# Performance work log

Measured on AMD Instinct MI355X. Metric: run time of the kernel, lower is better.

The kernel has to match this reference:

```python
import jax, jax.numpy as jnp
import numpy as np
import math

C = 16
K = 16
M = 64
DEPTH = 4          # int(sqrt(K)) tree depth
D = C * 9          # input feature dim, 9 dims per codebook subspace
N = 1024 * 128     # rows
N_NODES = K - 1    # 15 internal nodes of a depth-4 binary tree


def _selection_matrix(C):
    # node i at tree level l reads the per-codebook hashed feature at depth index l
    S = np.zeros((C * N_NODES, C * DEPTH), np.float32)
    for c in range(C):
        for i in range(N_NODES):
            level = 0 if i == 0 else (1 if i < 3 else (2 if i < 7 else 3))
            S[c * N_NODES + i, c * DEPTH + level] = 1.0
    return S


def _bit_matrix(C, K):
    # row (c,k): +/-1 on the 4 tree nodes along code k's root-to-leaf path;
    # matching code scores DEPTH, every other code scores <= DEPTH-2
    B = np.zeros((C * K, C * N_NODES), np.float32)
    for c in range(C):
        for k in range(K):
            prefix = 0
            for l in range(DEPTH):
                bit = (k >> (DEPTH - 1 - l)) & 1
                node = (2 ** l - 1) + prefix
                B[c * K + k, c * N_NODES + node] = 1.0 if bit else -1.0
                prefix = prefix * 2 + bit
    return B


def setup_inputs() -> dict:
    key = jax.random.key(0)
    k1, k2, k3, k4 = jax.random.split(key, 4)
    I = jax.random.normal(k1, (N, D), jnp.float32) - 0.5
    A = jax.random.normal(k2, (C, D // C, DEPTH), jnp.float32)   # soft hashing projections
    T = jax.random.normal(k3, (C * N_NODES,), jnp.float32)       # node thresholds
    bound = math.sqrt(1.0 / (C * K))  # kaiming_uniform with a=sqrt(5), fan_in=C*K
    L = jax.random.uniform(k4, (M, C, K), jnp.float32, -bound, bound)  # lookup tables
    S = jnp.asarray(_selection_matrix(C))
    B = jnp.asarray(_bit_matrix(C, K))
    return {"I": I, "A": A, "T": T, "L": L, "S": S, "B": B}


def reference(I, A, T, L, S, B):
    n = I.shape[0]
    # per-codebook soft hash: (n, C, D//C) x (C, D//C, DEPTH) -> (n, C*DEPTH)
    h = jnp.einsum('ncd,cdp->ncp', I.reshape(n, C, D // C), A).reshape(n, C * DEPTH)
    # thresholded tree decisions with straight-through sign
    b = h @ S.T - T                                   # (n, C*15)
    t = jnp.tanh(b)
    s = jax.lax.stop_gradient(jnp.sign(b) - t) + t    # fwd: sign, bwd: tanh'
    # bit-matrix decode of path agreements -> per-code scores
    scores = (s @ B.T).reshape(n, C, K)               # (n, C, K), max DEPTH at true code
    onehot = jax.nn.one_hot(jnp.argmax(scores, axis=2), K, dtype=I.dtype)
    E = jax.lax.stop_gradient(onehot - scores) + scores  # STE one-hot encoding
    # LUT gather-accumulate: out[n,m] = sum_c L[m,c,code(n,c)]
    return jnp.einsum('nck,mck->nm', E, L)
```

## Files before the change

kernel.cpp:

```cpp
#include <hip/hip_runtime.h>
#include <hip/hip_fp16.h>


#define NROWS (1024 * 128)

typedef __attribute__((ext_vector_type(2))) float f32x2;

__global__ __launch_bounds__(256, 2) void halut_fwd(
    const float* __restrict__ I,
    const float* __restrict__ A,
    const float* __restrict__ T,
    const float* __restrict__ L,
    float* __restrict__ out)
{
    __shared__ uint32_t sLut[8192];
    __shared__ float    sStage[4][2304];
    __shared__ uint8_t  sCodes[4096];

    const int tid  = threadIdx.x;
    const int w    = tid >> 6;
    const int lane = tid & 63;

    const int cB = lane & 15;
    const int g  = lane >> 4;
    f32x2 a01[9], a23[9];
    {
        const float4* ap4 = (const float4*)(A + cB * 36);
        #pragma unroll
        for (int i = 0; i < 9; ++i) {
            const float4 v = ap4[i];
            a01[i] = (f32x2){v.x, v.y};
            a23[i] = (f32x2){v.z, v.w};
        }
    }
    float Tf[15];
    #pragma unroll
    for (int j = 0; j < 15; ++j) Tf[j] = T[cB * 15 + j];

    {
        uint4* lut4 = (uint4*)sLut;
        #pragma unroll
        for (int q = 0; q < 8; ++q) {
            uint32_t wv[4];
            #pragma unroll
            for (int e = 0; e < 4; ++e) {
                const float fa = L[(8*q + 2*e)     * 256 + tid];
                const float fb = L[(8*q + 2*e + 1) * 256 + tid];
                wv[e] = ((uint32_t)__half_as_ushort(__float2half_rn(fb)) << 16)
                      |  (uint32_t)__half_as_ushort(__float2half_rn(fa));
            }
            lut4[q * 256 + tid] = make_uint4(wv[0], wv[1], wv[2], wv[3]);
        }
    }
    __syncthreads();

    const int wave_row0 = blockIdx.x * 256 + w * 64;
    const float4* Isrc = (const float4*)I;
    float4* st4 = (float4*)sStage[w];

    float4 nbuf[9];
    #pragma unroll
    for (int i = 0; i < 9; ++i)
        nbuf[i] = Isrc[(size_t)wave_row0 * 36 + i * 64 + lane];

    const int lvl[15] = {0, 1,1, 2,2,2,2, 3,3,3,3,3,3,3,3};

    #pragma unroll
    for (int p16 = 0; p16 < 4; ++p16) {
        #pragma unroll
        for (int i = 0; i < 9; ++i) st4[i * 64 + lane] = nbuf[i];
        if (p16 < 3) {
            #pragma unroll
            for (int i = 0; i < 9; ++i)
                nbuf[i] = Isrc[(size_t)(wave_row0 + (p16+1)*16) * 36 + i*64 + lane];
        }
        #pragma unroll
        for (int ps = 0; ps < 4; ++ps) {
            const int lr = ps * 4 + g;
            const float* xr = &sStage[w][lr * 144 + cB * 9];

            float xv[9];
            f32x2 h01 = (f32x2){0.f, 0.f}, h23 = (f32x2){0.f, 0.f};
            #pragma unroll
            for (int d = 0; d < 9; ++d) {
                const float x = xr[d];
                xv[d] = x;
                const f32x2 xx = (f32x2){x, x};
                h01 = __builtin_elementwise_fma(xx, a01[d], h01);
                h23 = __builtin_elementwise_fma(xx, a23[d], h23);
            }
            const float hh[4] = {h01.x, h01.y, h23.x, h23.y};

            uint32_t mk = 0, bl = 0;
            #pragma unroll
            for (int j = 0; j < 15; ++j) {
                const float b = hh[lvl[j]] - Tf[j];
                mk |= (b > 0.f) ? (1u << j) : 0u;
                bl |= (fabsf(b) < 1e-3f) ? 1u : 0u;
            }
            if (bl) {
                double h0 = 0.0, h1 = 0.0, h2 = 0.0, h3 = 0.0;
                #pragma unroll
                for (int d = 0; d < 9; ++d) {
                    const double x = (double)xv[d];
                    h0 = fma(x, (double)a01[d].x, h0);
                    h1 = fma(x, (double)a01[d].y, h1);
                    h2 = fma(x, (double)a23[d].x, h2);
                    h3 = fma(x, (double)a23[d].y, h3);
                }
                const double hd[4] = {h0, h1, h2, h3};
                mk = 0;
                #pragma unroll
                for (int j = 0; j < 15; ++j)
                    mk |= (hd[lvl[j]] > (double)Tf[j]) ? (1u << j) : 0u;
            }
            int p =       (int)(mk & 1u);
            p = 2 * p + (int)((mk >> (1 + p)) & 1u);
            p = 2 * p + (int)((mk >> (3 + p)) & 1u);
            p = 2 * p + (int)((mk >> (7 + p)) & 1u);
            sCodes[(w * 64 + p16 * 16 + lr) * 16 + cB] = (uint8_t)p;
        }
    }

    const uint4 cw = *(const uint4*)&sCodes[tid * 16];
    const uint32_t cd0 = cw.x, cd1 = cw.y, cd2 = cw.z, cd3 = cw.w;

    __half2 acc2[32];
    #pragma unroll
    for (int k = 0; k < 32; ++k) acc2[k] = __floats2half2_rn(0.f, 0.f);

    const uint4* lut4 = (const uint4*)sLut;
    #pragma unroll 4
    for (int c = 0; c < 16; ++c) {
        const uint32_t cdw = (c < 4) ? cd0 : (c < 8) ? cd1 : (c < 12) ? cd2 : cd3;
        const int p = (int)((cdw >> ((c & 3) * 8)) & 15u);
        const uint4* colp = lut4 + (c << 4) + p;
        #pragma unroll
        for (int q = 0; q < 8; ++q) {
            const uint4 wv = colp[q << 8];
            acc2[q*4+0] = __hadd2(acc2[q*4+0], *(const __half2*)&wv.x);
            acc2[q*4+1] = __hadd2(acc2[q*4+1], *(const __half2*)&wv.y);
            acc2[q*4+2] = __hadd2(acc2[q*4+2], *(const __half2*)&wv.z);
            acc2[q*4+3] = __hadd2(acc2[q*4+3], *(const __half2*)&wv.w);
        }
    }

    __syncthreads();
    float* sO = (float*)sLut;
    #pragma unroll
    for (int half = 0; half < 2; ++half) {
        if ((tid >> 7) == half) {
            const int r = tid & 127;
            #pragma unroll
            for (int ch = 0; ch < 16; ++ch) {
                const float4 v = make_float4(__low2float (acc2[2 * ch]),
                                             __high2float(acc2[2 * ch]),
                                             __low2float (acc2[2 * ch + 1]),
                                             __high2float(acc2[2 * ch + 1]));
                *(float4*)&sO[(r << 6) + ((ch ^ (r & 15)) << 2)] = v;
            }
        }
        __syncthreads();
        float4* op = (float4*)(out + (size_t)blockIdx.x * (256 * 64)
                                   + (size_t)half * (128 * 64));
        #pragma unroll
        for (int j = 0; j < 8; ++j) {
            const int F  = tid + (j << 8);
            const int r2 = F >> 4;
            const int m2 = F & 15;
            op[F] = *(const float4*)&sO[(r2 << 6) + ((m2 ^ (r2 & 15)) << 2)];
        }
        __syncthreads();
    }
}

extern "C" void kernel_launch(void* const* d_in, const int* in_sizes, int n_in,
                              void* d_out, int out_size, void* d_ws, size_t ws_size,
                              hipStream_t stream) {
    const float* I = (const float*)d_in[0];
    const float* A = (const float*)d_in[1];
    const float* T = (const float*)d_in[2];
    const float* L = (const float*)d_in[3];
    float* outp = (float*)d_out;

    const int nblocks = NROWS / 256;
    halut_fwd<<<nblocks, 256, 0, stream>>>(I, A, T, L, outp);
}
```

Baseline: 28.65 us.

## Halve rows per block, drop LDS input staging, split LUT accumulation across thread pairs

Each block now handles 128 rows instead of 256, with two threads per row each accumulating half of the 64 outputs. This halves the fp16 accumulator registers, and launch bounds are raised to allow 4 blocks per CU. Input rows are no longer staged through shared memory. Each lane reads its 9 floats directly from global memory with a double-buffered register prefetch, and codes are packed via shuffles into 32-bit words. This cuts LDS use and raises occupancy, but gives up the fully coalesced float4 input loads and makes each block rebuild the LUT in LDS twice as often in total.

After: 69.44 us. 142% more time.

```diff
diff --git a/kernel.cpp b/kernel.cpp
--- a/kernel.cpp
+++ b/kernel.cpp
@@ -6,7 +6,7 @@
 
 typedef __attribute__((ext_vector_type(2))) float f32x2;
 
-__global__ __launch_bounds__(256, 2) void halut_fwd(
+__global__ __launch_bounds__(256, 4) void halut_fwd(
     const float* __restrict__ I,
     const float* __restrict__ A,
     const float* __restrict__ T,
@@ -14,15 +14,14 @@
     float* __restrict__ out)
 {
     __shared__ uint32_t sLut[8192];
-    __shared__ float    sStage[4][2304];
-    __shared__ uint8_t  sCodes[4096];
+    __shared__ uint32_t sCodes[512];
 
     const int tid  = threadIdx.x;
     const int w    = tid >> 6;
     const int lane = tid & 63;
+    const int cB   = lane & 15;
+    const int g    = lane >> 4;
 
-    const int cB = lane & 15;
-    const int g  = lane >> 4;
     f32x2 a01[9], a23[9];
     {
         const float4* ap4 = (const float4*)(A + cB * 36);
@@ -38,139 +37,130 @@
     for (int j = 0; j < 15; ++j) Tf[j] = T[cB * 15 + j];
 
     {
-        uint4* lut4 = (uint4*)sLut;
+        uint4* dst = (uint4*)sLut;
         #pragma unroll
-        for (int q = 0; q < 8; ++q) {
+        for (int i = 0; i < 8; ++i) {
             uint32_t wv[4];
             #pragma unroll
-            for (int e = 0; e < 4; ++e) {
-                const float fa = L[(8*q + 2*e)     * 256 + tid];
-                const float fb = L[(8*q + 2*e + 1) * 256 + tid];
-                wv[e] = ((uint32_t)__half_as_ushort(__float2half_rn(fb)) << 16)
-                      |  (uint32_t)__half_as_ushort(__float2half_rn(fa));
+            for (int mh2 = 0; mh2 < 2; ++mh2) {
+                const int mb = mh2 * 32 + 4 * i;
+                const float fa = L[(mb + 0) * 256 + tid];
+                const float fb = L[(mb + 1) * 256 + tid];
+                const float fc = L[(mb + 2) * 256 + tid];
+                const float fd = L[(mb + 3) * 256 + tid];
+                wv[mh2*2+0] = ((uint32_t)__half_as_ushort(__float2half_rn(fb)) << 16)
+                            |  (uint32_t)__half_as_ushort(__float2half_rn(fa));
+                wv[mh2*2+1] = ((uint32_t)__half_as_ushort(__float2half_rn(fd)) << 16)
+                            |  (uint32_t)__half_as_ushort(__float2half_rn(fc));
             }
-            lut4[q * 256 + tid] = make_uint4(wv[0], wv[1], wv[2], wv[3]);
+            dst[i * 256 + tid] = make_uint4(wv[0], wv[1], wv[2], wv[3]);
         }
     }
     __syncthreads();
 
-    const int wave_row0 = blockIdx.x * 256 + w * 64;
-    const float4* Isrc = (const float4*)I;
-    float4* st4 = (float4*)sStage[w];
+    const int brow0 = blockIdx.x * 128;
+    const float* gb = I + (size_t)(brow0 + w * 32 + g) * 144 + cB * 9;
 
-    float4 nbuf[9];
+    float xb[2][9];
     #pragma unroll
-    for (int i = 0; i < 9; ++i)
-        nbuf[i] = Isrc[(size_t)wave_row0 * 36 + i * 64 + lane];
-
-    const int lvl[15] = {0, 1,1, 2,2,2,2, 3,3,3,3,3,3,3,3};
+    for (int d = 0; d < 9; ++d) xb[0][d] = gb[d];
 
     #pragma unroll
-    for (int p16 = 0; p16 < 4; ++p16) {
+    for (int ps = 0; ps < 8; ++ps) {
+        const float* xc = xb[ps & 1];
+        if (ps < 7) {
+            float* xn = xb[(ps + 1) & 1];
+            #pragma unroll
+            for (int d = 0; d < 9; ++d) xn[d] = gb[(ps + 1) * 576 + d];
+        }
+        f32x2 h01 = (f32x2){0.f, 0.f}, h23 = (f32x2){0.f, 0.f};
         #pragma unroll
-        for (int i = 0; i < 9; ++i) st4[i * 64 + lane] = nbuf[i];
-        if (p16 < 3) {
-            #pragma unroll
-            for (int i = 0; i < 9; ++i)
-                nbuf[i] = Isrc[(size_t)(wave_row0 + (p16+1)*16) * 36 + i*64 + lane];
+        for (int d = 0; d < 9; ++d) {
+            const f32x2 xx = (f32x2){xc[d], xc[d]};
+            h01 = __builtin_elementwise_fma(xx, a01[d], h01);
+            h23 = __builtin_elementwise_fma(xx, a23[d], h23);
         }
+        const float hh[4] = {h01.x, h01.y, h23.x, h23.y};
+        uint32_t mk = 0, bl = 0;
         #pragma unroll
-        for (int ps = 0; ps < 4; ++ps) {
-            const int lr = ps * 4 + g;
-            const float* xr = &sStage[w][lr * 144 + cB * 9];
-
-            float xv[9];
-            f32x2 h01 = (f32x2){0.f, 0.f}, h23 = (f32x2){0.f, 0.f};
+        for (int j = 0; j < 15; ++j) {
+            const int lv = (j == 0) ? 0 : (j < 3) ? 1 : (j < 7) ? 2 : 3;
+            const float b = hh[lv] - Tf[j];
+            mk |= (b > 0.f) ? (1u << j) : 0u;
+            bl |= (fabsf(b) < 1e-3f) ? 1u : 0u;
+        }
+        if (bl) {
+            double h0 = 0.0, h1 = 0.0, h2 = 0.0, h3 = 0.0;
             #pragma unroll
             for (int d = 0; d < 9; ++d) {
-                const float x = xr[d];
-                xv[d] = x;
-                const f32x2 xx = (f32x2){x, x};
-                h01 = __builtin_elementwise_fma(xx, a01[d], h01);
-                h23 = __builtin_elementwise_fma(xx, a23[d], h23);
+                const double x = (double)xc[d];
+                h0 = fma(x, (double)a01[d].x, h0);
+                h1 = fma(x, (double)a01[d].y, h1);
+                h2 = fma(x, (double)a23[d].x, h2);
+                h3 = fma(x, (double)a23[d].y, h3);
             }
-            const float hh[4] = {h01.x, h01.y, h23.x, h23.y};
-
-            uint32_t mk = 0, bl = 0;
+            const double hd[4] = {h0, h1, h2, h3};
+            mk = 0;
             #pragma unroll
             for (int j = 0; j < 15; ++j) {
-                const float b = hh[lvl[j]] - Tf[j];
-                mk |= (b > 0.f) ? (1u << j) : 0u;
-                bl |= (fabsf(b) < 1e-3f) ? 1u : 0u;
+                const int lv = (j == 0) ? 0 : (j < 3) ? 1 : (j < 7) ? 2 : 3;
+                mk |= (hd[lv] > (double)Tf[j]) ? (1u << j) : 0u;
             }
-            if (bl) {
-                double h0 = 0.0, h1 = 0.0, h2 = 0.0, h3 = 0.0;
-                #pragma unroll
-                for (int d = 0; d < 9; ++d) {
-                    const double x = (double)xv[d];
-                    h0 = fma(x, (double)a01[d].x, h0);
-                    h1 = fma(x, (double)a01[d].y, h1);
-                    h2 = fma(x, (double)a23[d].x, h2);
-                    h3 = fma(x, (double)a23[d].y, h3);
-                }
-                const double hd[4] = {h0, h1, h2, h3};
-                mk = 0;
-                #pragma unroll
-                for (int j = 0; j < 15; ++j)
-                    mk |= (hd[lvl[j]] > (double)Tf[j]) ? (1u << j) : 0u;
-            }
-            int p =       (int)(mk & 1u);
-            p = 2 * p + (int)((mk >> (1 + p)) & 1u);
-            p = 2 * p + (int)((mk >> (3 + p)) & 1u);
-            p = 2 * p + (int)((mk >> (7 + p)) & 1u);
-            sCodes[(w * 64 + p16 * 16 + lr) * 16 + cB] = (uint8_t)p;
         }
+        int p =       (int)(mk & 1u);
+        p = 2 * p + (int)((mk >> (1 + p)) & 1u);
+        p = 2 * p + (int)((mk >> (3 + p)) & 1u);
+        p = 2 * p + (int)((mk >> (7 + p)) & 1u);
+
+        uint32_t v = (uint32_t)p << (8 * (cB & 3));
+        v |= __shfl_xor(v, 1);
+        v |= __shfl_xor(v, 2);
+        if ((lane & 3) == 0)
+            sCodes[(w * 32 + ps * 4 + g) * 4 + (cB >> 2)] = v;
     }
 
-    const uint4 cw = *(const uint4*)&sCodes[tid * 16];
-    const uint32_t cd0 = cw.x, cd1 = cw.y, cd2 = cw.z, cd3 = cw.w;
+    const int lr = tid >> 1;
+    const int mh = tid & 1;
+    const uint4 cw = ((const uint4*)sCodes)[lr];
 
-    __half2 acc2[32];
+    __half2 acc2[16];
     #pragma unroll
-    for (int k = 0; k < 32; ++k) acc2[k] = __floats2half2_rn(0.f, 0.f);
+    for (int k = 0; k < 16; ++k) acc2[k] = __floats2half2_rn(0.f, 0.f);
 
-    const uint4* lut4 = (const uint4*)sLut;
+    const uint2* lut2 = (const uint2*)sLut;
     #pragma unroll 4
     for (int c = 0; c < 16; ++c) {
-        const uint32_t cdw = (c < 4) ? cd0 : (c < 8) ? cd1 : (c < 12) ? cd2 : cd3;
-        const int p = (int)((cdw >> ((c & 3) * 8)) & 15u);
-        const uint4* colp = lut4 + (c << 4) + p;
+        const uint32_t cdw = (c < 4) ? cw.x : (c < 8) ? cw.y : (c < 12) ? cw.z : cw.w;
+        const int p    = (int)((cdw >> ((c & 3) * 8)) & 15u);
+        const int col2 = (c * 16 + p) * 2 + mh;
         #pragma unroll
-        for (int q = 0; q < 8; ++q) {
-            const uint4 wv = colp[q << 8];
-            acc2[q*4+0] = __hadd2(acc2[q*4+0], *(const __half2*)&wv.x);
-            acc2[q*4+1] = __hadd2(acc2[q*4+1], *(const __half2*)&wv.y);
-            acc2[q*4+2] = __hadd2(acc2[q*4+2], *(const __half2*)&wv.z);
-            acc2[q*4+3] = __hadd2(acc2[q*4+3], *(const __half2*)&wv.w);
+        for (int i = 0; i < 8; ++i) {
+            const uint2 uv = lut2[i * 512 + col2];
+            acc2[2*i]   = __hadd2(acc2[2*i],   *(const __half2*)&uv.x);
+            acc2[2*i+1] = __hadd2(acc2[2*i+1], *(const __half2*)&uv.y);
         }
     }
 
     __syncthreads();
     float* sO = (float*)sLut;
     #pragma unroll
-    for (int half = 0; half < 2; ++half) {
-        if ((tid >> 7) == half) {
-            const int r = tid & 127;
-            #pragma unroll
-            for (int ch = 0; ch < 16; ++ch) {
-                const float4 v = make_float4(__low2float (acc2[2 * ch]),
-                                             __high2float(acc2[2 * ch]),
-                                             __low2float (acc2[2 * ch + 1]),
-                                             __high2float(acc2[2 * ch + 1]));
-                *(float4*)&sO[(r << 6) + ((ch ^ (r & 15)) << 2)] = v;
-            }
-        }
-        __syncthreads();
-        float4* op = (float4*)(out + (size_t)blockIdx.x * (256 * 64)
-                                   + (size_t)half * (128 * 64));
-        #pragma unroll
-        for (int j = 0; j < 8; ++j) {
-            const int F  = tid + (j << 8);
-            const int r2 = F >> 4;
-            const int m2 = F & 15;
-            op[F] = *(const float4*)&sO[(r2 << 6) + ((m2 ^ (r2 & 15)) << 2)];
-        }
-        __syncthreads();
+    for (int k2 = 0; k2 < 8; ++k2) {
+        const int ch = mh * 8 + k2;
+        const float4 v = make_float4(__low2float (acc2[2*k2]),
+                                     __high2float(acc2[2*k2]),
+                                     __low2float (acc2[2*k2+1]),
+                                     __high2float(acc2[2*k2+1]));
+        *(float4*)&sO[(lr << 6) + ((ch ^ (lr & 15)) << 2)] = v;
+    }
+    __syncthreads();
+
+    float4* op = (float4*)(out + (size_t)blockIdx.x * (128 * 64));
+    #pragma unroll
+    for (int j = 0; j < 8; ++j) {
+        const int F  = tid + (j << 8);
+        const int r2 = F >> 4;
+        const int m2 = F & 15;
+        op[F] = *(const float4*)&sO[(r2 << 6) + ((m2 ^ (r2 & 15)) << 2)];
     }
 }
 
@@ -183,6 +173,6 @@
     const float* L = (const float*)d_in[3];
     float* outp = (float*)d_out;
 
-    const int nblocks = NROWS / 256;
+    const int nblocks = NROWS / 128;
     halut_fwd<<<nblocks, 256, 0, stream>>>(I, A, T, L, outp);
 }
```
